# Optimization experiments

Hardware: AMD Instinct MI355X
Metric: run time of the kernel (lower is better)

Reference implementation:

```python
import jax, jax.numpy as jnp
import numpy as np

H, W = 1024, 1024
NUM_FEATURES = 64
NUM_PILLARS = 100000


def setup_inputs() -> dict:
    key = jax.random.key(0)
    k1, k2 = jax.random.split(key)
    pillar_features = jax.random.normal(k1, (NUM_PILLARS, NUM_FEATURES), dtype=jnp.float32)
    coords = jax.random.randint(k2, (NUM_PILLARS, 3), 0, 1024, dtype=jnp.int64)
    return {"pillar_features": pillar_features, "coords": coords}


def reference(pillar_features, coords):
    # pillar_features: [N, F]; coords: [N, 3] = (batch_idx, y_idx, x_idx)
    x_idx = coords[:, 2]
    y_idx = coords[:, 1]
    valid = (x_idx >= 0) & (x_idx < W) & (y_idx >= 0) & (y_idx < H)
    # Flatten spatial dims; route invalid pillars to an out-of-bounds slot
    # that mode='drop' discards (matches the torch valid_mask filtering).
    flat_idx = jnp.where(valid, y_idx * W + x_idx, H * W)
    img = jnp.zeros((NUM_FEATURES, H * W), dtype=pillar_features.dtype)
    # single vectorized scatter: [F, N] updates into [F, H*W]
    img = img.at[:, flat_idx].set(pillar_features.T, mode='drop')
    return img.reshape(1, NUM_FEATURES, H, W)
```

## Files before the change

kernel.cpp:

```cpp
#include <hip/hip_runtime.h>


constexpr int H    = 1024;
constexpr int W    = 1024;
constexpr int HW   = H * W;
constexpr int NF   = 64;
constexpr int TILE = 256;
constexpr int HALF = 32;

__global__ void winner_kernel(const int* __restrict__ coords,
                              int* __restrict__ winner, int np) {
    int p = blockIdx.x * blockDim.x + threadIdx.x;
    if (p >= np) return;
    int y = coords[p * 3 + 1];
    int x = coords[p * 3 + 2];
    if ((unsigned)x < (unsigned)W && (unsigned)y < (unsigned)H) {
        atomicMax(winner + (y * W + x), p);
    }
}

__global__ void __launch_bounds__(256, 4) fill_kernel(const float* __restrict__ feat,
                                                      const int* __restrict__ winner,
                                                      float* __restrict__ out) {
    __shared__ float lds[HALF * TILE];

    const int base = blockIdx.x * TILE;
    const int t    = threadIdx.x;
    const int wv   = t >> 6;
    const int l    = t & 63;

    const int wp = winner[base + t];

    {
        float4 z = {0.0f, 0.0f, 0.0f, 0.0f};
#pragma unroll
        for (int j = 0; j < 8; ++j)
            *(float4*)&lds[j * 1024 + t * 4] = z;
    }
    __syncthreads();

    const float4* row = (const float4*)(feat + (size_t)max(wp, 0) * NF);

    for (int h = 0; h < 2; ++h) {
        if (wp >= 0) {
#pragma unroll
            for (int j = 0; j < 8; ++j) {
                float4 r = row[h * 8 + j];
                lds[(j * 4 + 0) * TILE + t] = r.x;
                lds[(j * 4 + 1) * TILE + t] = r.y;
                lds[(j * 4 + 2) * TILE + t] = r.z;
                lds[(j * 4 + 3) * TILE + t] = r.w;
            }
        }
        __syncthreads();

#pragma unroll
        for (int p = 0; p < 8; ++p) {
            const int floc = p * 4 + wv;
            float4 v = *(const float4*)&lds[floc * TILE + l * 4];
            *(float4*)(out + (size_t)(h * HALF + floc) * HW + base + l * 4) = v;
        }
        __syncthreads();
    }
}

extern "C" void kernel_launch(void* const* d_in, const int* in_sizes, int n_in,
                              void* d_out, int out_size, void* d_ws, size_t ws_size,
                              hipStream_t stream) {
    const float* feat   = (const float*)d_in[0];
    const int*   coords = (const int*)d_in[1];
    float*       out    = (float*)d_out;
    int np = in_sizes[1] / 3;

    int* winner = (int*)d_ws;

    (void)hipMemsetAsync(winner, 0xFF, (size_t)HW * sizeof(int), stream);
    winner_kernel<<<(np + 255) / 256, 256, 0, stream>>>(coords, winner, np);
    fill_kernel<<<HW / TILE, 256, 0, stream>>>(feat, winner, out);
}
```

Measured before the change: 309.0 us.

## Widen fill tile to 1024 pixels and stage features in eight-channel passes

The fill kernel now gives each 256-thread block 1024 output pixels, so every thread handles four winner indices. Features are staged through LDS in eight passes of eight channels each, instead of two passes of 32. This cuts the block count and lengthens the contiguous output run each wave writes per channel plane to 4 KB. In exchange there are more barrier rounds per block and more scattered 32-byte feature reads per pass. LDS use stays at 32 KB.

```diff
diff --git a/kernel.cpp b/kernel.cpp
--- a/kernel.cpp
+++ b/kernel.cpp
@@ -1,12 +1,13 @@
 #include <hip/hip_runtime.h>
 
 
-constexpr int H    = 1024;
-constexpr int W    = 1024;
-constexpr int HW   = H * W;
-constexpr int NF   = 64;
-constexpr int TILE = 256;
-constexpr int HALF = 32;
+constexpr int H     = 1024;
+constexpr int W     = 1024;
+constexpr int HW    = H * W;
+constexpr int NF    = 64;
+constexpr int TILE  = 1024;
+constexpr int FP    = 8;
+constexpr int NPASS = NF / FP;
 
 __global__ void winner_kernel(const int* __restrict__ coords,
                               int* __restrict__ winner, int np) {
@@ -19,17 +20,30 @@
     }
 }
 
+__device__ __forceinline__ void stage8(const float4* __restrict__ row, int q,
+                                       float* __restrict__ lds, int c) {
+    float4 a = row[q * 2 + 0];
+    float4 b = row[q * 2 + 1];
+    lds[0 * TILE + c] = a.x;  lds[1 * TILE + c] = a.y;
+    lds[2 * TILE + c] = a.z;  lds[3 * TILE + c] = a.w;
+    lds[4 * TILE + c] = b.x;  lds[5 * TILE + c] = b.y;
+    lds[6 * TILE + c] = b.z;  lds[7 * TILE + c] = b.w;
+}
+
 __global__ void __launch_bounds__(256, 4) fill_kernel(const float* __restrict__ feat,
                                                       const int* __restrict__ winner,
                                                       float* __restrict__ out) {
-    __shared__ float lds[HALF * TILE];
+    __shared__ float lds[FP * TILE];
 
     const int base = blockIdx.x * TILE;
     const int t    = threadIdx.x;
     const int wv   = t >> 6;
     const int l    = t & 63;
 
-    const int wp = winner[base + t];
+    const int w0 = winner[base + t];
+    const int w1 = winner[base + t + 256];
+    const int w2 = winner[base + t + 512];
+    const int w3 = winner[base + t + 768];
 
     {
         float4 z = {0.0f, 0.0f, 0.0f, 0.0f};
@@ -39,26 +53,27 @@
     }
     __syncthreads();
 
-    const float4* row = (const float4*)(feat + (size_t)max(wp, 0) * NF);
+    const float4* r0 = (const float4*)(feat + (size_t)max(w0, 0) * NF);
+    const float4* r1 = (const float4*)(feat + (size_t)max(w1, 0) * NF);
+    const float4* r2 = (const float4*)(feat + (size_t)max(w2, 0) * NF);
+    const float4* r3 = (const float4*)(feat + (size_t)max(w3, 0) * NF);
 
-    for (int h = 0; h < 2; ++h) {
-        if (wp >= 0) {
-#pragma unroll
-            for (int j = 0; j < 8; ++j) {
-                float4 r = row[h * 8 + j];
-                lds[(j * 4 + 0) * TILE + t] = r.x;
-                lds[(j * 4 + 1) * TILE + t] = r.y;
-                lds[(j * 4 + 2) * TILE + t] = r.z;
-                lds[(j * 4 + 3) * TILE + t] = r.w;
-            }
-        }
+    for (int q = 0; q < NPASS; ++q) {
+        if (w0 >= 0) stage8(r0, q, lds, t);
+        if (w1 >= 0) stage8(r1, q, lds, t + 256);
+        if (w2 >= 0) stage8(r2, q, lds, t + 512);
+        if (w3 >= 0) stage8(r3, q, lds, t + 768);
         __syncthreads();
 
 #pragma unroll
-        for (int p = 0; p < 8; ++p) {
-            const int floc = p * 4 + wv;
-            float4 v = *(const float4*)&lds[floc * TILE + l * 4];
-            *(float4*)(out + (size_t)(h * HALF + floc) * HW + base + l * 4) = v;
+        for (int pl = 0; pl < 2; ++pl) {
+            const int floc = wv * 2 + pl;
+            float* op = out + (size_t)(q * FP + floc) * HW + base;
+#pragma unroll
+            for (int ch = 0; ch < 4; ++ch) {
+                float4 v = *(const float4*)&lds[floc * TILE + ch * 256 + l * 4];
+                *(float4*)(op + ch * 256 + l * 4) = v;
+            }
         }
         __syncthreads();
     }
```

Measured after the change: 300.1 us. 2.9% less time.
